# Performance work log

Measured on AMD Instinct MI355X. Metric: run time of the kernel, lower is better.

Reference implementation:

```python
import jax, jax.numpy as jnp
import numpy as np

GROUPS = 32
EPS = 1e-5
NUM_HEADS = 8

def group_norm(x, w, b):
    # x: [B, C, H, W], normalize over (C//G, H, W) per group
    B, C, H, W = x.shape
    xg = x.reshape(B, GROUPS, C // GROUPS, H, W)
    mean = xg.mean(axis=(2, 3, 4), keepdims=True)
    var = xg.var(axis=(2, 3, 4), keepdims=True)
    xg = (xg - mean) * jax.lax.rsqrt(var + EPS)
    x = xg.reshape(B, C, H, W)
    return x * w[None, :, None, None] + b[None, :, None, None]

def setup_inputs() -> dict:
    key = jax.random.key(0)
    ks = jax.random.split(key, 3)
    C = 512
    x = jax.random.normal(ks[0], (8, C, 32, 32), dtype=jnp.float32)
    gn_w = jnp.ones((C,), jnp.float32)
    gn_b = jnp.zeros((C,), jnp.float32)
    # 1x1 conv weights stored as [out, in] matrices
    qkv_w = jax.random.normal(ks[1], (3 * C, C), dtype=jnp.float32) * (C ** -0.5)
    qkv_b = jnp.zeros((3 * C,), jnp.float32)
    proj_w = jax.random.normal(ks[2], (C, C), dtype=jnp.float32) * (C ** -0.5)
    proj_b = jnp.zeros((C,), jnp.float32)
    return {"x": x, "gn_w": gn_w, "gn_b": gn_b, "qkv_w": qkv_w,
            "qkv_b": qkv_b, "proj_w": proj_w, "proj_b": proj_b}

def reference(x, gn_w, gn_b, qkv_w, qkv_b, proj_w, proj_b):
    B, C, H, W = x.shape
    nh = NUM_HEADS
    hd = C // nh
    N = H * W
    residual = x
    xn = group_norm(x, gn_w, gn_b)
    # 1x1 conv == channel matmul: [B, 3C, H, W]
    qkv = jnp.einsum('bchw,oc->bohw', xn, qkv_w) + qkv_b[None, :, None, None]
    # [B, 3, nh, hd, N] -> q/k/v each [B, nh, N, hd]
    qkv = qkv.reshape(B, 3, nh, hd, N).transpose(1, 0, 2, 4, 3)
    q, k, v = qkv[0], qkv[1], qkv[2]
    scale = hd ** -0.5
    attn = jnp.einsum('bhqd,bhkd->bhqk', q, k) * scale
    attn = jax.nn.softmax(attn, axis=-1)
    out = jnp.einsum('bhqk,bhkd->bhqd', attn, v)  # [B, nh, N, hd]
    out = out.transpose(0, 1, 3, 2).reshape(B, C, H, W)
    out = jnp.einsum('bchw,oc->bohw', out, proj_w) + proj_b[None, :, None, None]
    return out + residual
```

## Files before the change

### kernel.cpp

```cpp
#include <hip/hip_runtime.h>


typedef __bf16 bf16;
typedef __bf16 bf16x8 __attribute__((ext_vector_type(8)));
typedef __bf16 bf16x4 __attribute__((ext_vector_type(4)));
typedef float  f32x4  __attribute__((ext_vector_type(4)));
typedef float  f32x16 __attribute__((ext_vector_type(16)));
typedef unsigned u32x4 __attribute__((ext_vector_type(4)));

#define MFMA_16x16x32(A, B, C) __builtin_amdgcn_mfma_f32_16x16x32_bf16((A), (B), (C), 0, 0, 0)
#define MFMA_32x32x16(A, B, C) __builtin_amdgcn_mfma_f32_32x32x16_bf16((A), (B), (C), 0, 0, 0)

static __device__ __forceinline__ unsigned cvt_pk_bf16(float a, float b) {
  unsigned r;
  asm("v_cvt_pk_bf16_f32 %0, %1, %2" : "=v"(r) : "v"(a), "v"(b));
  return r;
}

static __device__ __forceinline__ void async_stage_128x32(
    const bf16* __restrict__ g0, bf16* lds, int tid) {
  const int wv = tid >> 6, ln = tid & 63;
#pragma unroll
  for (int cc = 0; cc < 2; ++cc) {
    const int c = wv + cc * 4;
    const bf16* g = g0 + (size_t)(c * 16 + (ln >> 2)) * 512 + (ln & 3) * 8;
    __builtin_amdgcn_global_load_lds(
        (const __attribute__((address_space(1))) void*)g,
        (__attribute__((address_space(3))) void*)(lds + c * 512),
        16, 0, 0);
  }
}

static __device__ __forceinline__ void async_stage_64x32(
    const bf16* __restrict__ g0, bf16* lds, int tid) {
  const int wv = tid >> 6, ln = tid & 63;
  const bf16* g = g0 + (size_t)(wv * 16 + (ln >> 2)) * 512 + (ln & 3) * 8;
  __builtin_amdgcn_global_load_lds(
      (const __attribute__((address_space(1))) void*)g,
      (__attribute__((address_space(3))) void*)(lds + wv * 512),
      16, 0, 0);
}

__global__ __launch_bounds__(256) void gn_fused_kernel(
    const float* __restrict__ x,
    const float* __restrict__ gn_w, const float* __restrict__ gn_b,
    const float* __restrict__ qw, const float* __restrict__ pw,
    bf16* __restrict__ wq, bf16* __restrict__ wp, bf16* __restrict__ xn_t) {
  const int t = threadIdx.x;
  if (blockIdx.x >= 256) {
    const int idx = (blockIdx.x - 256) * 256 + t;
    if (idx < 196608) {
      float4 v = ((const float4*)qw)[idx];
      bf16x4 o = { (bf16)v.x, (bf16)v.y, (bf16)v.z, (bf16)v.w };
      *(bf16x4*)(&wq[idx * 4]) = o;
    }
    if (idx < 65536) {
      float4 v = ((const float4*)pw)[idx];
      bf16x4 o = { (bf16)v.x, (bf16)v.y, (bf16)v.z, (bf16)v.w };
      *(bf16x4*)(&wp[idx * 4]) = o;
    }
    return;
  }
  const int bg = blockIdx.x;
  const int b = bg >> 5, g = bg & 31;
  const int c0 = g * 16;
  const float4* p = (const float4*)(x + ((size_t)b * 512 + c0) * 1024);
  float4 v[16];
  float s = 0.f, s2 = 0.f;
#pragma unroll
  for (int i = 0; i < 16; ++i) {
    v[i] = p[t + 256 * i];
    s  += (v[i].x + v[i].y) + (v[i].z + v[i].w);
    s2 += (v[i].x * v[i].x + v[i].y * v[i].y) + (v[i].z * v[i].z + v[i].w * v[i].w);
  }
#pragma unroll
  for (int d = 1; d < 64; d <<= 1) {
    s  += __shfl_xor(s,  d);
    s2 += __shfl_xor(s2, d);
  }
  __shared__ float as[4], as2[4];
  __shared__ float scs[16], shs[16];
  if ((t & 63) == 0) { as[t >> 6] = s; as2[t >> 6] = s2; }
  __syncthreads();
  if (t < 16) {
    float S  = as[0] + as[1] + as[2] + as[3];
    float S2 = as2[0] + as2[1] + as2[2] + as2[3];
    float m  = S * (1.0f / 16384.0f);
    float rs = rsqrtf(S2 * (1.0f / 16384.0f) - m * m + 1e-5f);
    float sc = rs * gn_w[c0 + t];
    scs[t] = sc;
    shs[t] = gn_b[c0 + t] - m * sc;
  }
  __syncthreads();
  bf16* ob = xn_t + ((size_t)b * 1024 + 4 * t) * 512 + c0;
#pragma unroll
  for (int j = 0; j < 4; ++j) {
    bf16 tmp[16];
#pragma unroll
    for (int i = 0; i < 16; ++i) {
      float val = (j == 0) ? v[i].x : (j == 1) ? v[i].y : (j == 2) ? v[i].z : v[i].w;
      tmp[i] = (bf16)(val * scs[i] + shs[i]);
    }
    *(bf16x8*)(ob + (size_t)j * 512)     = *(bf16x8*)(tmp);
    *(bf16x8*)(ob + (size_t)j * 512 + 8) = *(bf16x8*)(tmp + 8);
  }
}

__global__ __launch_bounds__(256) void qkv_gemm_kernel(
    const bf16* __restrict__ W, const bf16* __restrict__ xn_t,
    const float* __restrict__ qkv_b, bf16* __restrict__ qkv_t,
    bf16* __restrict__ v_t) {
  const int n0 = blockIdx.x * 128;
  const int o0 = blockIdx.y * 128;
  const int b  = blockIdx.z;
  __shared__ bf16 As[2][128 * 32];
  __shared__ bf16 Bs[2][128 * 32];
  const int tid = threadIdx.x, ln = tid & 63, wv = tid >> 6;
  const int mw = (wv >> 1) * 64, nw = (wv & 1) * 64;
  const int l15 = ln & 15, lg = ln >> 4;
  const bool isV = (o0 >= 1024);
  const bf16* gA = W + (size_t)o0 * 512;
  const bf16* gB = xn_t + ((size_t)b * 1024 + n0) * 512;
  f32x4 acc[4][4] = {};
  async_stage_128x32(gA, As[0], tid);
  async_stage_128x32(gB, Bs[0], tid);
  for (int it = 0; it < 16; ++it) {
    __syncthreads();
    const int cur = it & 1, nxt = cur ^ 1;
    if (it < 15) {
      async_stage_128x32(gA + (it + 1) * 32, As[nxt], tid);
      async_stage_128x32(gB + (it + 1) * 32, Bs[nxt], tid);
    }
    bf16x8 af[4], bfr[4];
#pragma unroll
    for (int mi = 0; mi < 4; ++mi)
      af[mi] = *(const bf16x8*)(&As[cur][(mw + mi * 16 + l15) * 32 + lg * 8]);
#pragma unroll
    for (int nj = 0; nj < 4; ++nj)
      bfr[nj] = *(const bf16x8*)(&Bs[cur][(nw + nj * 16 + l15) * 32 + lg * 8]);
    if (!isV) {
#pragma unroll
      for (int mi = 0; mi < 4; ++mi)
#pragma unroll
        for (int nj = 0; nj < 4; ++nj)
          acc[mi][nj] = MFMA_16x16x32(af[mi], bfr[nj], acc[mi][nj]);
    } else {
#pragma unroll
      for (int mi = 0; mi < 4; ++mi)
#pragma unroll
        for (int nj = 0; nj < 4; ++nj)
          acc[mi][nj] = MFMA_16x16x32(bfr[nj], af[mi], acc[mi][nj]);
    }
  }
  if (!isV) {
    const float qs = (o0 < 512) ? 0.125f * 1.44269504089f : 1.0f;
#pragma unroll
    for (int mi = 0; mi < 4; ++mi) {
      const int o = o0 + mw + mi * 16 + lg * 4;
      const float b0 = qkv_b[o], b1 = qkv_b[o + 1], b2 = qkv_b[o + 2], b3 = qkv_b[o + 3];
#pragma unroll
      for (int nj = 0; nj < 4; ++nj) {
        const int n = n0 + nw + nj * 16 + l15;
        f32x4 v = acc[mi][nj];
        bf16x4 st = { (bf16)((v.x + b0) * qs), (bf16)((v.y + b1) * qs),
                      (bf16)((v.z + b2) * qs), (bf16)((v.w + b3) * qs) };
        *(bf16x4*)(&qkv_t[((size_t)b * 1024 + n) * 1536 + o]) = st;
      }
    }
  } else {
#pragma unroll
    for (int mi = 0; mi < 4; ++mi) {
      const int o  = o0 + mw + mi * 16 + l15;
      const int hd = o - 1024;
      const float bias = qkv_b[o];
#pragma unroll
      for (int nj = 0; nj < 4; ++nj) {
        const int n = n0 + nw + nj * 16 + lg * 4;
        f32x4 v = acc[mi][nj];
        bf16x4 st = { (bf16)(v.x + bias), (bf16)(v.y + bias),
                      (bf16)(v.z + bias), (bf16)(v.w + bias) };
        *(bf16x4*)(&v_t[((size_t)b * 512 + hd) * 1024 + n]) = st;
      }
    }
  }
}

__global__ __launch_bounds__(512, 4) void attn_kernel(
    const bf16* __restrict__ qkv_t, const bf16* __restrict__ v_t,
    bf16* __restrict__ at_t) {
  const int qt = blockIdx.y;
  const int b  = blockIdx.x >> 3;
  const int h  = blockIdx.x & 7;
  __shared__ __align__(16) char smem[73728];
  const int tid = threadIdx.x, ln = tid & 63, wv = tid >> 6;
  const int half = wv >> 2, w4 = wv & 3;
  const int l31 = ln & 31, hi = ln >> 5;
  const bf16* hq  = qkv_t + (size_t)b * 1024 * 1536 + h * 64;
  const bf16* hk  = hq + 512;
  const bf16* vtb = v_t + (size_t)(b * 8 + h) * 64 * 1024;

  const int qb = qt * 128 + w4 * 32;
  bf16x8 qf[4];
#pragma unroll
  for (int ks = 0; ks < 4; ++ks)
    qf[ks] = *(const bf16x8*)(hq + (size_t)(qb + l31) * 1536 + ks * 16 + hi * 8);

  f32x16 oacc[2] = {};
  float lst = 0.f;

  const int t256 = tid & 255;
  const int srow = t256 >> 2, scg = (t256 & 3) * 16;
  const int kt0 = half * 8;

  bf16x8 s0, s1, s2, s3;
  {
    const bf16* gk = hk  + (size_t)(kt0 * 64 + srow) * 1536 + scg;
    const bf16* gv = vtb + (size_t)srow * 1024 + kt0 * 64 + scg;
    s0 = *(const bf16x8*)(gk);
    s1 = *(const bf16x8*)(gk + 8);
    s2 = *(const bf16x8*)(gv);
    s3 = *(const bf16x8*)(gv + 8);
    bf16* Kt = (bf16*)(smem + half * 18432);
    bf16* Vt = Kt + 64 * 72;
    *(bf16x8*)(&Kt[srow * 72 + scg])     = s0;
    *(bf16x8*)(&Kt[srow * 72 + scg + 8]) = s1;
    *(bf16x8*)(&Vt[srow * 72 + scg])     = s2;
    *(bf16x8*)(&Vt[srow * 72 + scg + 8]) = s3;
  }

  for (int i = 0; i < 8; ++i) {
    __syncthreads();
    if (i < 7) {
      const int kt = kt0 + i + 1;
      const bf16* gk = hk  + (size_t)(kt * 64 + srow) * 1536 + scg;
      const bf16* gv = vtb + (size_t)srow * 1024 + kt * 64 + scg;
      s0 = *(const bf16x8*)(gk);
      s1 = *(const bf16x8*)(gk + 8);
      s2 = *(const bf16x8*)(gv);
      s3 = *(const bf16x8*)(gv + 8);
    }
    const bf16* Kt = (const bf16*)(smem + (i & 1) * 36864 + half * 18432);
    const bf16* Vt = Kt + 64 * 72;

#pragma unroll
    for (int kk = 0; kk < 2; ++kk) {
      const int kvb = kk * 32;
      f32x16 st = {};
#pragma unroll
      for (int ks = 0; ks < 4; ++ks) {
        bf16x8 kf = *(const bf16x8*)(&Kt[(kvb + l31) * 72 + ks * 16 + hi * 8]);
        st = MFMA_32x32x16(kf, qf[ks], st);
      }
#pragma unroll
      for (int r = 0; r < 16; ++r) st[r] = exp2f(st[r]);
      lst += ((st[0] + st[1]) + (st[2] + st[3])) + ((st[4] + st[5]) + (st[6] + st[7]))
           + ((st[8] + st[9]) + (st[10] + st[11])) + ((st[12] + st[13]) + (st[14] + st[15]));
#pragma unroll
      for (int t = 0; t < 2; ++t) {
        unsigned x0 = cvt_pk_bf16(st[t * 8 + 0], st[t * 8 + 1]);
        unsigned x1 = cvt_pk_bf16(st[t * 8 + 2], st[t * 8 + 3]);
        unsigned y0 = cvt_pk_bf16(st[t * 8 + 4], st[t * 8 + 5]);
        unsigned y1 = cvt_pk_bf16(st[t * 8 + 6], st[t * 8 + 7]);
        asm("v_permlane32_swap_b32 %0, %1" : "+v"(x0), "+v"(y0));
        asm("v_permlane32_swap_b32 %0, %1" : "+v"(x1), "+v"(y1));
        u32x4 pu = { x0, x1, y0, y1 };
        bf16x8 pb = __builtin_bit_cast(bf16x8, pu);
#pragma unroll
        for (int dt = 0; dt < 2; ++dt) {
          bf16x8 vf = *(const bf16x8*)(&Vt[(dt * 32 + l31) * 72 + kvb + t * 16 + hi * 8]);
          oacc[dt] = MFMA_32x32x16(vf, pb, oacc[dt]);
        }
      }
    }

    if (i < 7) {
      bf16* Ktn = (bf16*)(smem + ((i + 1) & 1) * 36864 + half * 18432);
      bf16* Vtn = Ktn + 64 * 72;
      *(bf16x8*)(&Ktn[srow * 72 + scg])     = s0;
      *(bf16x8*)(&Ktn[srow * 72 + scg + 8]) = s1;
      *(bf16x8*)(&Vtn[srow * 72 + scg])     = s2;
      *(bf16x8*)(&Vtn[srow * 72 + scg + 8]) = s3;
    }
  }

  const float lf = lst + __shfl_xor(lst, 32);

  float* MB  = (float*)smem;
  float* MLb = (float*)(smem + 34816);
  __syncthreads();
  if (half == 1) {
    float* mb = MB + w4 * (32 * 68);
#pragma unroll
    for (int dt = 0; dt < 2; ++dt)
#pragma unroll
      for (int rr = 0; rr < 4; ++rr) {
        f32x4 v = { oacc[dt][rr * 4 + 0], oacc[dt][rr * 4 + 1],
                    oacc[dt][rr * 4 + 2], oacc[dt][rr * 4 + 3] };
        *(f32x4*)(mb + l31 * 68 + dt * 32 + rr * 8 + hi * 4) = v;
      }
    if (hi == 0) MLb[w4 * 32 + l31] = lf;
  }
  __syncthreads();
  if (half == 0) {
    const float* mb = MB + w4 * (32 * 68);
    const float inv = 1.0f / (lf + MLb[w4 * 32 + l31]);
    const int q = qb + l31;
#pragma unroll
    for (int dt = 0; dt < 2; ++dt)
#pragma unroll
      for (int rr = 0; rr < 4; ++rr) {
        f32x4 ob = *(const f32x4*)(mb + l31 * 68 + dt * 32 + rr * 8 + hi * 4);
        bf16x4 ov = { (bf16)((oacc[dt][rr * 4 + 0] + ob[0]) * inv),
                      (bf16)((oacc[dt][rr * 4 + 1] + ob[1]) * inv),
                      (bf16)((oacc[dt][rr * 4 + 2] + ob[2]) * inv),
                      (bf16)((oacc[dt][rr * 4 + 3] + ob[3]) * inv) };
        *(bf16x4*)(&at_t[((size_t)b * 1024 + q) * 512 + h * 64 + dt * 32 + rr * 8 + hi * 4]) = ov;
      }
  }
}

__global__ __launch_bounds__(256) void proj_gemm_kernel(
    const bf16* __restrict__ at_t, const bf16* __restrict__ wp,
    const float* __restrict__ proj_b, const float* __restrict__ x,
    float* __restrict__ out) {
  const int i0 = blockIdx.x * 64;
  const int c0 = blockIdx.y * 128;
  const int b  = blockIdx.z;
  __shared__ bf16 As[2][64 * 32];
  __shared__ bf16 Bs[2][128 * 32];
  const int tid = threadIdx.x, ln = tid & 63, wv = tid >> 6;
  const int mw = (wv >> 1) * 32, nw = (wv & 1) * 64;
  const int l15 = ln & 15, lg = ln >> 4;
  const bf16* gA = at_t + ((size_t)b * 1024 + i0) * 512;
  const bf16* gB = wp + (size_t)c0 * 512;
  f32x4 acc[2][4] = {};
  async_stage_64x32(gA, As[0], tid);
  async_stage_128x32(gB, Bs[0], tid);
  for (int it = 0; it < 16; ++it) {
    __syncthreads();
    const int cur = it & 1, nxt = cur ^ 1;
    if (it < 15) {
      async_stage_64x32(gA + (it + 1) * 32, As[nxt], tid);
      async_stage_128x32(gB + (it + 1) * 32, Bs[nxt], tid);
    }
    bf16x8 af[2], bfr[4];
#pragma unroll
    for (int mi = 0; mi < 2; ++mi)
      af[mi] = *(const bf16x8*)(&As[cur][(mw + mi * 16 + l15) * 32 + lg * 8]);
#pragma unroll
    for (int nj = 0; nj < 4; ++nj)
      bfr[nj] = *(const bf16x8*)(&Bs[cur][(nw + nj * 16 + l15) * 32 + lg * 8]);
#pragma unroll
    for (int mi = 0; mi < 2; ++mi)
#pragma unroll
      for (int nj = 0; nj < 4; ++nj)
        acc[mi][nj] = MFMA_16x16x32(af[mi], bfr[nj], acc[mi][nj]);
  }
#pragma unroll
  for (int mi = 0; mi < 2; ++mi) {
    const int i = i0 + mw + mi * 16 + lg * 4;
#pragma unroll
    for (int nj = 0; nj < 4; ++nj) {
      const int c = c0 + nw + nj * 16 + l15;
      const float bias = proj_b[c];
      const size_t off = ((size_t)b * 512 + c) * 1024 + i;
      const float4 res = *(const float4*)(x + off);
      f32x4 v = acc[mi][nj];
      float4 ov;
      ov.x = v.x + bias + res.x;
      ov.y = v.y + bias + res.y;
      ov.z = v.z + bias + res.z;
      ov.w = v.w + bias + res.w;
      *(float4*)(out + off) = ov;
    }
  }
}

extern "C" void kernel_launch(void* const* d_in, const int* in_sizes, int n_in,
                              void* d_out, int out_size, void* d_ws, size_t ws_size,
                              hipStream_t stream) {
  (void)in_sizes; (void)n_in; (void)out_size; (void)ws_size;
  const float* x      = (const float*)d_in[0];
  const float* gn_w   = (const float*)d_in[1];
  const float* gn_b   = (const float*)d_in[2];
  const float* qkv_w  = (const float*)d_in[3];
  const float* qkv_b  = (const float*)d_in[4];
  const float* proj_w = (const float*)d_in[5];
  const float* proj_b = (const float*)d_in[6];
  float* out = (float*)d_out;

  char* ws = (char*)d_ws;
  bf16* wq    = (bf16*)ws;
  bf16* wp    = wq + (size_t)1536 * 512;
  bf16* xn_t  = wp + (size_t)512 * 512;
  bf16* qkv_t = xn_t + (size_t)8 * 1024 * 512;
  bf16* at_t  = qkv_t + (size_t)8 * 1024 * 1536;
  bf16* v_t   = at_t + (size_t)8 * 1024 * 512;

  hipLaunchKernelGGL(gn_fused_kernel, dim3(1280),     dim3(256), 0, stream,
                     x, gn_w, gn_b, qkv_w, proj_w, wq, wp, xn_t);
  hipLaunchKernelGGL(qkv_gemm_kernel, dim3(8, 12, 8), dim3(256), 0, stream,
                     wq, xn_t, qkv_b, qkv_t, v_t);
  hipLaunchKernelGGL(attn_kernel,     dim3(64, 8),    dim3(512), 0, stream,
                     qkv_t, v_t, at_t);
  hipLaunchKernelGGL(proj_gemm_kernel,dim3(16, 4, 8), dim3(256), 0, stream,
                     at_t, wp, proj_b, x, out);
}
```

Baseline: 154.2 us.

## Drop KV split in attention, use 4 waves per block with priority hints

The attention kernel previously split the 16 KV tiles across two wave groups of 512 threads and merged their partial outputs through LDS at the end. It now uses 256 threads, each wave walks all 16 KV tiles, and the LDS merge and its extra barriers are gone, which also halves shared memory per block. s_setprio is raised around the MFMA sections to favour matrix issue. The trade-off is a longer serial KV loop per wave and half the waves per query tile, so less latency hiding within a block, offset by more blocks able to fit per CU.

New measurement: 157.2 us. Within noise of the previous version (+1.9%).

```diff
diff --git a/kernel.cpp b/kernel.cpp
--- a/kernel.cpp
+++ b/kernel.cpp
@@ -185,21 +185,21 @@
   }
 }
 
-__global__ __launch_bounds__(512, 4) void attn_kernel(
+__global__ __launch_bounds__(256, 2) void attn_kernel(
     const bf16* __restrict__ qkv_t, const bf16* __restrict__ v_t,
     bf16* __restrict__ at_t) {
   const int qt = blockIdx.y;
   const int b  = blockIdx.x >> 3;
   const int h  = blockIdx.x & 7;
-  __shared__ __align__(16) char smem[73728];
-  const int tid = threadIdx.x, ln = tid & 63, wv = tid >> 6;
-  const int half = wv >> 2, w4 = wv & 3;
+  __shared__ __align__(16) char smem[36864];
+  const int tid = threadIdx.x, wv = tid >> 6;
+  const int ln = tid & 63;
   const int l31 = ln & 31, hi = ln >> 5;
   const bf16* hq  = qkv_t + (size_t)b * 1024 * 1536 + h * 64;
   const bf16* hk  = hq + 512;
   const bf16* vtb = v_t + (size_t)(b * 8 + h) * 64 * 1024;
 
-  const int qb = qt * 128 + w4 * 32;
+  const int qb = qt * 128 + wv * 32;
   bf16x8 qf[4];
 #pragma unroll
   for (int ks = 0; ks < 4; ++ks)
@@ -208,49 +208,50 @@
   f32x16 oacc[2] = {};
   float lst = 0.f;
 
-  const int t256 = tid & 255;
-  const int srow = t256 >> 2, scg = (t256 & 3) * 16;
-  const int kt0 = half * 8;
-
-  bf16x8 s0, s1, s2, s3;
+  const int srow = tid >> 3;
+  const int scol = (tid & 7) * 8;
+
+  bf16x8 k0, k1, v0, v1;
   {
-    const bf16* gk = hk  + (size_t)(kt0 * 64 + srow) * 1536 + scg;
-    const bf16* gv = vtb + (size_t)srow * 1024 + kt0 * 64 + scg;
-    s0 = *(const bf16x8*)(gk);
-    s1 = *(const bf16x8*)(gk + 8);
-    s2 = *(const bf16x8*)(gv);
-    s3 = *(const bf16x8*)(gv + 8);
-    bf16* Kt = (bf16*)(smem + half * 18432);
+    const bf16* gk = hk + (size_t)srow * 1536 + scol;
+    const bf16* gv = vtb + (size_t)srow * 1024 + scol;
+    k0 = *(const bf16x8*)(gk);
+    k1 = *(const bf16x8*)(gk + 32 * 1536);
+    v0 = *(const bf16x8*)(gv);
+    v1 = *(const bf16x8*)(gv + 32 * 1024);
+    bf16* Kt = (bf16*)(smem);
     bf16* Vt = Kt + 64 * 72;
-    *(bf16x8*)(&Kt[srow * 72 + scg])     = s0;
-    *(bf16x8*)(&Kt[srow * 72 + scg + 8]) = s1;
-    *(bf16x8*)(&Vt[srow * 72 + scg])     = s2;
-    *(bf16x8*)(&Vt[srow * 72 + scg + 8]) = s3;
-  }
-
-  for (int i = 0; i < 8; ++i) {
+    *(bf16x8*)(&Kt[srow * 72 + scol])        = k0;
+    *(bf16x8*)(&Kt[(srow + 32) * 72 + scol]) = k1;
+    *(bf16x8*)(&Vt[srow * 72 + scol])        = v0;
+    *(bf16x8*)(&Vt[(srow + 32) * 72 + scol]) = v1;
+  }
+
+  for (int i = 0; i < 16; ++i) {
     __syncthreads();
-    if (i < 7) {
-      const int kt = kt0 + i + 1;
-      const bf16* gk = hk  + (size_t)(kt * 64 + srow) * 1536 + scg;
-      const bf16* gv = vtb + (size_t)srow * 1024 + kt * 64 + scg;
-      s0 = *(const bf16x8*)(gk);
-      s1 = *(const bf16x8*)(gk + 8);
-      s2 = *(const bf16x8*)(gv);
-      s3 = *(const bf16x8*)(gv + 8);
-    }
-    const bf16* Kt = (const bf16*)(smem + (i & 1) * 36864 + half * 18432);
+    if (i < 15) {
+      const int kt = i + 1;
+      const bf16* gk = hk  + (size_t)(kt * 64 + srow) * 1536 + scol;
+      const bf16* gv = vtb + (size_t)srow * 1024 + kt * 64 + scol;
+      k0 = *(const bf16x8*)(gk);
+      k1 = *(const bf16x8*)(gk + 32 * 1536);
+      v0 = *(const bf16x8*)(gv);
+      v1 = *(const bf16x8*)(gv + 32 * 1024);
+    }
+    const bf16* Kt = (const bf16*)(smem + (i & 1) * 18432);
     const bf16* Vt = Kt + 64 * 72;
 
 #pragma unroll
     for (int kk = 0; kk < 2; ++kk) {
       const int kvb = kk * 32;
       f32x16 st = {};
+      __builtin_amdgcn_s_setprio(1);
 #pragma unroll
       for (int ks = 0; ks < 4; ++ks) {
         bf16x8 kf = *(const bf16x8*)(&Kt[(kvb + l31) * 72 + ks * 16 + hi * 8]);
         st = MFMA_32x32x16(kf, qf[ks], st);
       }
+      __builtin_amdgcn_s_setprio(0);
 #pragma unroll
       for (int r = 0; r < 16; ++r) st[r] = exp2f(st[r]);
       lst += ((st[0] + st[1]) + (st[2] + st[3])) + ((st[4] + st[5]) + (st[6] + st[7]))
@@ -265,58 +266,40 @@
         asm("v_permlane32_swap_b32 %0, %1" : "+v"(x1), "+v"(y1));
         u32x4 pu = { x0, x1, y0, y1 };
         bf16x8 pb = __builtin_bit_cast(bf16x8, pu);
+        __builtin_amdgcn_s_setprio(1);
 #pragma unroll
         for (int dt = 0; dt < 2; ++dt) {
           bf16x8 vf = *(const bf16x8*)(&Vt[(dt * 32 + l31) * 72 + kvb + t * 16 + hi * 8]);
           oacc[dt] = MFMA_32x32x16(vf, pb, oacc[dt]);
         }
+        __builtin_amdgcn_s_setprio(0);
       }
     }
 
-    if (i < 7) {
-      bf16* Ktn = (bf16*)(smem + ((i + 1) & 1) * 36864 + half * 18432);
+    if (i < 15) {
+      bf16* Ktn = (bf16*)(smem + ((i + 1) & 1) * 18432);
       bf16* Vtn = Ktn + 64 * 72;
-      *(bf16x8*)(&Ktn[srow * 72 + scg])     = s0;
-      *(bf16x8*)(&Ktn[srow * 72 + scg + 8]) = s1;
-      *(bf16x8*)(&Vtn[srow * 72 + scg])     = s2;
-      *(bf16x8*)(&Vtn[srow * 72 + scg + 8]) = s3;
+      *(bf16x8*)(&Ktn[srow * 72 + scol])        = k0;
+      *(bf16x8*)(&Ktn[(srow + 32) * 72 + scol]) = k1;
+      *(bf16x8*)(&Vtn[srow * 72 + scol])        = v0;
+      *(bf16x8*)(&Vtn[(srow + 32) * 72 + scol]) = v1;
     }
   }
 
   const float lf = lst + __shfl_xor(lst, 32);
-
-  float* MB  = (float*)smem;
-  float* MLb = (float*)(smem + 34816);
-  __syncthreads();
-  if (half == 1) {
-    float* mb = MB + w4 * (32 * 68);
-#pragma unroll
-    for (int dt = 0; dt < 2; ++dt)
-#pragma unroll
-      for (int rr = 0; rr < 4; ++rr) {
-        f32x4 v = { oacc[dt][rr * 4 + 0], oacc[dt][rr * 4 + 1],
-                    oacc[dt][rr * 4 + 2], oacc[dt][rr * 4 + 3] };
-        *(f32x4*)(mb + l31 * 68 + dt * 32 + rr * 8 + hi * 4) = v;
-      }
-    if (hi == 0) MLb[w4 * 32 + l31] = lf;
-  }
-  __syncthreads();
-  if (half == 0) {
-    const float* mb = MB + w4 * (32 * 68);
-    const float inv = 1.0f / (lf + MLb[w4 * 32 + l31]);
-    const int q = qb + l31;
-#pragma unroll
-    for (int dt = 0; dt < 2; ++dt)
-#pragma unroll
-      for (int rr = 0; rr < 4; ++rr) {
-        f32x4 ob = *(const f32x4*)(mb + l31 * 68 + dt * 32 + rr * 8 + hi * 4);
-        bf16x4 ov = { (bf16)((oacc[dt][rr * 4 + 0] + ob[0]) * inv),
-                      (bf16)((oacc[dt][rr * 4 + 1] + ob[1]) * inv),
-                      (bf16)((oacc[dt][rr * 4 + 2] + ob[2]) * inv),
-                      (bf16)((oacc[dt][rr * 4 + 3] + ob[3]) * inv) };
-        *(bf16x4*)(&at_t[((size_t)b * 1024 + q) * 512 + h * 64 + dt * 32 + rr * 8 + hi * 4]) = ov;
-      }
-  }
+  const float inv = 1.0f / lf;
+  const int q = qb + l31;
+  bf16* ob = at_t + ((size_t)b * 1024 + q) * 512 + h * 64;
+#pragma unroll
+  for (int dt = 0; dt < 2; ++dt)
+#pragma unroll
+    for (int rr = 0; rr < 4; ++rr) {
+      bf16x4 ov = { (bf16)(oacc[dt][rr * 4 + 0] * inv),
+                    (bf16)(oacc[dt][rr * 4 + 1] * inv),
+                    (bf16)(oacc[dt][rr * 4 + 2] * inv),
+                    (bf16)(oacc[dt][rr * 4 + 3] * inv) };
+      *(bf16x4*)(ob + dt * 32 + rr * 8 + hi * 4) = ov;
+    }
 }
 
 __global__ __launch_bounds__(256) void proj_gemm_kernel(
@@ -401,7 +384,7 @@
                      x, gn_w, gn_b, qkv_w, proj_w, wq, wp, xn_t);
   hipLaunchKernelGGL(qkv_gemm_kernel, dim3(8, 12, 8), dim3(256), 0, stream,
                      wq, xn_t, qkv_b, qkv_t, v_t);
-  hipLaunchKernelGGL(attn_kernel,     dim3(64, 8),    dim3(512), 0, stream,
+  hipLaunchKernelGGL(attn_kernel,     dim3(64, 8),    dim3(256), 0, stream,
                      qkv_t, v_t, at_t);
   hipLaunchKernelGGL(proj_gemm_kernel,dim3(16, 4, 8), dim3(256), 0, stream,
                      at_t, wp, proj_b, x, out);
```
